# Kernel tuning notes

Hardware: AMD Instinct MI355X
Metric: run time of the kernel (lower is better)

The kernel has to match this reference:

```python
import jax, jax.numpy as jnp
import numpy as np
import math

D_MODEL = 512
HEADS = 8
GRID_COUNT = 40000
MAX_LEN = 5000


def _positional_embedding(d_model, max_len=MAX_LEN):
    pe = np.zeros((max_len, d_model), dtype=np.float32)
    position = np.arange(max_len, dtype=np.float32)[:, None]
    div_term = np.exp(np.arange(0, d_model, 2, dtype=np.float32) * -(math.log(10000.0) / d_model))
    pe[:, 0::2] = np.sin(position * div_term)
    pe[:, 1::2] = np.cos(position * div_term)
    return jnp.asarray(pe)  # [max_len, d_model]


def _mha(q, k, v, wq, bq, wk, bk, wv, bv, heads):
    # Faithful to SelfAttention: no 1/sqrt(d_k) scaling in the original.
    B, Sq, D = q.shape
    Sk = k.shape[1]
    dh = D // heads
    Q = (q @ wq.T + bq).reshape(B, Sq, heads, dh)
    K = (k @ wk.T + bk).reshape(B, Sk, heads, dh)
    V = (v @ wv.T + bv).reshape(B, Sk, heads, dh)
    attn = jax.nn.softmax(jnp.einsum('bqhd,bkhd->bhqk', Q, K), axis=-1)
    out = jnp.einsum('bhqk,bkhd->bqhd', attn, V)
    return out.reshape(B, Sq, D)


def setup_inputs() -> dict:
    key = jax.random.key(0)
    ks = jax.random.split(key, 20)
    B, S_CURR, S_HIST, N_MASK = 32, 128, 256, 16
    s = 1.0 / math.sqrt(D_MODEL)

    def lin(k):
        kw, kb = jax.random.split(k)
        w = jax.random.uniform(kw, (D_MODEL, D_MODEL), jnp.float32, -s, s)
        b = jax.random.uniform(kb, (D_MODEL,), jnp.float32, -s, s)
        return w, b

    h_wq, h_bq = lin(ks[0]); h_wk, h_bk = lin(ks[1]); h_wv, h_bv = lin(ks[2])
    c_wq, c_bq = lin(ks[3]); c_wk, c_bk = lin(ks[4]); c_wv, c_bv = lin(ks[5])
    x_wq, x_bq = lin(ks[6]); x_wk, x_bk = lin(ks[7]); x_wv, x_bv = lin(ks[8])
    t2_w, t2_b = lin(ks[9])
    emb = jax.random.normal(ks[10], (GRID_COUNT, D_MODEL), jnp.float32)

    return {
        'hist_traj_grid': jax.random.randint(ks[11], (B, S_HIST), 0, GRID_COUNT),
        'userId': jax.random.randint(ks[12], (B,), 0, 1000),
        'mask_pos': jax.random.randint(ks[13], (B, N_MASK), 0, S_CURR),
        'mask_curr_traj_grid': jax.random.randint(ks[14], (B, S_CURR), 0, GRID_COUNT),
        'aggregator_hist_traj_grid': jax.random.randint(ks[15], (B, S_HIST), 0, GRID_COUNT),
        'emb': emb,
        'h_wq': h_wq, 'h_bq': h_bq, 'h_wk': h_wk, 'h_bk': h_bk, 'h_wv': h_wv, 'h_bv': h_bv,
        'c_wq': c_wq, 'c_bq': c_bq, 'c_wk': c_wk, 'c_bk': c_bk, 'c_wv': c_wv, 'c_bv': c_bv,
        'x_wq': x_wq, 'x_bq': x_bq, 'x_wk': x_wk, 'x_bk': x_bk, 'x_wv': x_wv, 'x_bv': x_bv,
        't2_w': t2_w, 't2_b': t2_b,
    }


def reference(hist_traj_grid, userId, mask_pos, mask_curr_traj_grid, aggregator_hist_traj_grid,
              emb,
              h_wq, h_bq, h_wk, h_bk, h_wv, h_bv,
              c_wq, c_bq, c_wk, c_bk, c_wv, c_bv,
              x_wq, x_bq, x_wk, x_bk, x_wv, x_bv,
              t2_w, t2_b):
    pe = _positional_embedding(D_MODEL)
    hist = emb[aggregator_hist_traj_grid]          # [B, S_hist, D]
    curr = emb[mask_curr_traj_grid]                # [B, S_curr, D]
    hist = hist + pe[None, :hist.shape[1]]
    curr = curr + pe[None, :curr.shape[1]]

    hist = _mha(hist, hist, hist, h_wq, h_bq, h_wk, h_bk, h_wv, h_bv, HEADS)
    curr = _mha(curr, curr, curr, c_wq, c_bq, c_wk, c_bk, c_wv, c_bv, HEADS)
    _cross = _mha(curr, hist, hist, x_wq, x_bq, x_wk, x_bk, x_wv, x_bv, HEADS)
    # NOTE: original overwrites liner_transform output with liner_transform2(tanh(curr)),
    # so cross-attention output and liner_transform do not affect the result.
    hyb = jnp.tanh(curr) @ t2_w.T + t2_b           # [B, S_curr, D]

    # index_select of flattened [B*S, D] at mask_pos + b*S == take_along_axis over seq dim
    gathered = jnp.take_along_axis(hyb, mask_pos[:, :, None], axis=1)  # [B, n_mask, D]
    gathered = gathered.reshape(-1, D_MODEL)

    candidate = emb[2:]                            # [vocab-2, D]
    scores = gathered @ candidate.T                # [B*n_mask, vocab-2]
    return jax.nn.log_softmax(scores, axis=-1)
```

## Files before the change

### kernel.cpp

```cpp
#include <hip/hip_runtime.h>
#include <hip/hip_bf16.h>
#include <math.h>
#include <float.h>

#define B       32
#define S_CURR  128
#define D       512
#define H       8
#define DH      64
#define NM      16
#define NCAND   39998
#define MG      (B * NM)
#define SCLD    40064
#define NT      313

typedef __bf16 bf16x8_t __attribute__((ext_vector_type(8)));
typedef __bf16 bf16x4_t __attribute__((ext_vector_type(4)));
typedef __bf16 bf16x2_t __attribute__((ext_vector_type(2)));
typedef float  f32x4_t  __attribute__((ext_vector_type(4)));

typedef __attribute__((address_space(3))) unsigned int lds_u32_t;
typedef const __attribute__((address_space(1))) unsigned int gbl_u32_t;

__device__ __forceinline__ void async16(const void* g, void* l) {
    __builtin_amdgcn_global_load_lds((gbl_u32_t*)g, (lds_u32_t*)l, 16, 0, 0);
}

__global__ __launch_bounds__(256) void prep_kernel(
    const float* __restrict__ emb,
    const float* __restrict__ wq, const float* __restrict__ wk,
    const float* __restrict__ wv, const float* __restrict__ t2w,
    __bf16* __restrict__ embB, __bf16* __restrict__ wqB, __bf16* __restrict__ wkB,
    __bf16* __restrict__ wvB, __bf16* __restrict__ t2wB,
    const int* __restrict__ curr_idx, __bf16* __restrict__ currB,
    const int* __restrict__ mask_pos, int* __restrict__ qidx)
{
    int bx = blockIdx.x;
    if (bx < 10512) {
        const float* src; __bf16* dst; size_t n, base;
        if (bx < 10000) {
            src = emb + 2 * D; dst = embB; n = (size_t)NCAND * D; base = (size_t)bx * 2048;
        } else {
            int w = (bx - 10000) >> 7;
            base = (size_t)((bx - 10000) & 127) * 2048;
            n = (size_t)D * D;
            src = (w == 0) ? wq : (w == 1) ? wk : (w == 2) ? wv : t2w;
            dst = (w == 0) ? wqB : (w == 1) ? wkB : (w == 2) ? wvB : t2wB;
        }
        size_t i = base + (size_t)threadIdx.x * 8;
        if (i >= n) return;
        float4 a = *(const float4*)(src + i);
        float4 b = *(const float4*)(src + i + 4);
        bf16x8_t v;
        v[0] = (__bf16)a.x; v[1] = (__bf16)a.y; v[2] = (__bf16)a.z; v[3] = (__bf16)a.w;
        v[4] = (__bf16)b.x; v[5] = (__bf16)b.y; v[6] = (__bf16)b.z; v[7] = (__bf16)b.w;
        *(bf16x8_t*)(dst + i) = v;
        return;
    }
    if (bx == 14608) {
        int r = threadIdx.x;
        qidx[r] = (r >> 4) * S_CURR + mask_pos[r];
        r += 256;
        qidx[r] = (r >> 4) * S_CURR + mask_pos[r];
        return;
    }
    int bs = bx - 10512;
    int s = bs & (S_CURR - 1);
    int g = curr_idx[bs];
    const float* e = emb + (size_t)g * D;
    __bf16* o = currB + (size_t)bs * D;
    int d = threadIdx.x * 2;
    float div = __expf(-(float)d * (9.210340371976184f / 512.0f));
    float ang = (float)s * div;
    float2 ev = *(const float2*)(e + d);
    bf16x2_t ov;
    ov[0] = (__bf16)(ev.x + __sinf(ang));
    ov[1] = (__bf16)(ev.y + __cosf(ang));
    *(bf16x2_t*)(o + d) = ov;
}

__global__ __launch_bounds__(256) void gemm_bf(
    const __bf16* __restrict__ A,
    const __bf16* __restrict__ W0, const float* __restrict__ b0, __bf16* __restrict__ C0,
    const __bf16* __restrict__ W1, const float* __restrict__ b1, __bf16* __restrict__ C1,
    const __bf16* __restrict__ W2, const float* __restrict__ b2, __bf16* __restrict__ C2,
    const int* __restrict__ rowidx)
{
    const int z = blockIdx.z;
    if (z == 2 && blockIdx.x >= 4) return;
    const __bf16* W = (z == 0) ? W0 : (z == 1) ? W1 : W2;
    const float* bias = (z == 0) ? b0 : (z == 1) ? b1 : b2;
    __bf16* C = (z == 0) ? C0 : (z == 1) ? C1 : C2;

    __shared__ __bf16 As[2][128 * 64];
    __shared__ __bf16 Bs[2][128 * 64];

    const int tid = threadIdx.x, lane = tid & 63, wave = tid >> 6;
    const int wy = wave >> 1, wx = wave & 1;
    const int m0 = blockIdx.x * 128, n0 = blockIdx.y * 128;
    const int lrow = lane >> 3;
    const int lcol = (((lane & 7) ^ lrow) & 7) * 8;

    const __bf16* aptr[4]; const __bf16* bptr[4];
#pragma unroll
    for (int i = 0; i < 4; ++i) {
        int chunk = wave * 4 + i;
        int ar = m0 + chunk * 8 + lrow;
        if (z == 2) ar = rowidx[ar];
        aptr[i] = A + (size_t)ar * 512 + lcol;
        bptr[i] = W + (size_t)(n0 + chunk * 8 + lrow) * 512 + lcol;
    }

    f32x4_t acc[4][4];
#pragma unroll
    for (int i = 0; i < 4; ++i)
#pragma unroll
        for (int j = 0; j < 4; ++j) acc[i][j] = (f32x4_t){0.f, 0.f, 0.f, 0.f};

    const int l7 = lane & 7, quad = lane >> 4, c16 = lane & 15;

#pragma unroll
    for (int i = 0; i < 4; ++i) {
        int chunk = wave * 4 + i;
        async16(aptr[i], &As[0][chunk * 512]);
        async16(bptr[i], &Bs[0][chunk * 512]);
    }

#pragma unroll
    for (int t = 0; t < 8; ++t) {
        const int cur = t & 1;
        if (t < 7) {
            const int kk = (t + 1) * 64;
#pragma unroll
            for (int i = 0; i < 4; ++i) {
                int chunk = wave * 4 + i;
                async16(aptr[i] + kk, &As[cur ^ 1][chunk * 512]);
                async16(bptr[i] + kk, &Bs[cur ^ 1][chunk * 512]);
            }
            asm volatile("s_waitcnt vmcnt(8)" ::: "memory");
        } else {
            asm volatile("s_waitcnt vmcnt(0)" ::: "memory");
        }
        __builtin_amdgcn_s_barrier();
#pragma unroll
        for (int kb = 0; kb < 2; ++kb) {
            const int goff = (((kb * 4 + quad) ^ l7)) * 8;
            bf16x8_t af[4], bfv[4];
#pragma unroll
            for (int i = 0; i < 4; ++i)
                af[i] = *(const bf16x8_t*)&As[cur][(wy * 64 + i * 16 + c16) * 64 + goff];
#pragma unroll
            for (int j = 0; j < 4; ++j)
                bfv[j] = *(const bf16x8_t*)&Bs[cur][(wx * 64 + j * 16 + c16) * 64 + goff];
#pragma unroll
            for (int i = 0; i < 4; ++i)
#pragma unroll
                for (int j = 0; j < 4; ++j)
                    acc[i][j] = __builtin_amdgcn_mfma_f32_16x16x32_bf16(
                        bfv[j], af[i], acc[i][j], 0, 0, 0);
        }
        asm volatile("s_waitcnt lgkmcnt(0)" ::: "memory");
        __builtin_amdgcn_s_barrier();
    }

#pragma unroll
    for (int i = 0; i < 4; ++i) {
        const int row = m0 + wy * 64 + i * 16 + c16;
#pragma unroll
        for (int j = 0; j < 4; ++j) {
            const int colb = n0 + wx * 64 + j * 16 + quad * 4;
            float4 bv = *(const float4*)&bias[colb];
            bf16x4_t o;
            o[0] = (__bf16)(acc[i][j][0] + bv.x);
            o[1] = (__bf16)(acc[i][j][1] + bv.y);
            o[2] = (__bf16)(acc[i][j][2] + bv.z);
            o[3] = (__bf16)(acc[i][j][3] + bv.w);
            *(bf16x4_t*)&C[(size_t)row * 512 + colb] = o;
        }
    }
}

__global__ __launch_bounds__(256) void gemm_scores(
    const __bf16* __restrict__ A,
    const __bf16* __restrict__ Bm,
    __bf16* __restrict__ scB,
    float* __restrict__ pmax, float* __restrict__ psum)
{
    const int bid = blockIdx.x;
    const int xcd = bid & 7, k = bid >> 3;
    const int nt = xcd * 40 + (k >> 2);
    if (nt >= NT) return;
    const int m0 = (k & 3) * 128, n0 = nt * 128;

    __shared__ __bf16 As[2][128 * 32];
    __shared__ __bf16 Bs[2][128 * 32];
    __shared__ float redm[2][128], reds[2][128];

    const int tid = threadIdx.x, lane = tid & 63, wave = tid >> 6;
    const int wy = wave >> 1, wx = wave & 1;
    const int lrow16 = lane >> 2;
    const int pos    = lane & 3;
    const int quad = lane >> 4, c16 = lane & 15;

    const __bf16* aptr[2]; const __bf16* bptr[2]; int ldso[2];
#pragma unroll
    for (int i = 0; i < 2; ++i) {
        const int c = wave * 2 + i;
        const int g = pos ^ (lrow16 & 3) ^ (lrow16 >> 2);
        aptr[i] = A  + (size_t)(m0 + c * 16 + lrow16) * 512 + g * 8;
        bptr[i] = Bm + (size_t)(n0 + c * 16 + lrow16) * 512 + g * 8;
        ldso[i] = c * 512;
    }

    f32x4_t acc[4][4];
#pragma unroll
    for (int i = 0; i < 4; ++i)
#pragma unroll
        for (int j = 0; j < 4; ++j) acc[i][j] = (f32x4_t){0.f, 0.f, 0.f, 0.f};

#pragma unroll
    for (int i = 0; i < 2; ++i) {
        async16(aptr[i], &As[0][ldso[i]]);
        async16(bptr[i], &Bs[0][ldso[i]]);
    }

    const int goff = ((quad ^ (c16 & 3) ^ (c16 >> 2))) * 8;

#pragma unroll
    for (int t = 0; t < 16; ++t) {
        const int cur = t & 1;
        if (t < 15) {
            const int kk = (t + 1) * 32;
#pragma unroll
            for (int i = 0; i < 2; ++i) {
                async16(aptr[i] + kk, &As[cur ^ 1][ldso[i]]);
                async16(bptr[i] + kk, &Bs[cur ^ 1][ldso[i]]);
            }
            asm volatile("s_waitcnt vmcnt(4)" ::: "memory");
        } else {
            asm volatile("s_waitcnt vmcnt(0)" ::: "memory");
        }
        __builtin_amdgcn_s_barrier();
        bf16x8_t af[4], bfv[4];
#pragma unroll
        for (int i = 0; i < 4; ++i)
            af[i] = *(const bf16x8_t*)&As[cur][(wy * 64 + i * 16 + c16) * 32 + goff];
#pragma unroll
        for (int j = 0; j < 4; ++j)
            bfv[j] = *(const bf16x8_t*)&Bs[cur][(wx * 64 + j * 16 + c16) * 32 + goff];
#pragma unroll
        for (int i = 0; i < 4; ++i)
#pragma unroll
            for (int j = 0; j < 4; ++j)
                acc[i][j] = __builtin_amdgcn_mfma_f32_16x16x32_bf16(
                    bfv[j], af[i], acc[i][j], 0, 0, 0);
        asm volatile("s_waitcnt lgkmcnt(0)" ::: "memory");
        __builtin_amdgcn_s_barrier();
    }

    const bool tailb = (n0 + 128 > NCAND);
#pragma unroll
    for (int i = 0; i < 4; ++i) {
        const int lrw = wy * 64 + i * 16 + c16;
        const size_t rowbase = (size_t)(m0 + lrw) * SCLD;
        float vs[4][4];
        float vmax = -FLT_MAX;
        float ssum = 0.f;
        if (!tailb) {
#pragma unroll
            for (int j = 0; j < 4; ++j) {
                const int nb = n0 + wx * 64 + j * 16 + quad * 4;
                bf16x4_t o;
#pragma unroll
                for (int rr = 0; rr < 4; ++rr) {
                    __bf16 xb = (__bf16)acc[i][j][rr];
                    o[rr] = xb;
                    float xr = (float)xb;
                    vs[j][rr] = xr;
                    vmax = fmaxf(vmax, xr);
                }
                *(bf16x4_t*)&scB[rowbase + nb] = o;
            }
#pragma unroll
            for (int j = 0; j < 4; ++j)
#pragma unroll
                for (int rr = 0; rr < 4; ++rr)
                    ssum += __expf(vs[j][rr] - vmax);
        } else {
            for (int j = 0; j < 4; ++j) {
                const int nb = n0 + wx * 64 + j * 16 + quad * 4;
                for (int rr = 0; rr < 4; ++rr) {
                    const int n = nb + rr;
                    __bf16 xb = (__bf16)acc[i][j][rr];
                    float xr = (float)xb;
                    if (n < NCAND) {
                        scB[rowbase + n] = xb;
                        vs[j][rr] = xr;
                        vmax = fmaxf(vmax, xr);
                    } else vs[j][rr] = -FLT_MAX;
                }
            }
            for (int j = 0; j < 4; ++j)
                for (int rr = 0; rr < 4; ++rr)
                    ssum += (vs[j][rr] > -FLT_MAX) ? __expf(vs[j][rr] - vmax) : 0.f;
        }
#pragma unroll
        for (int mk = 16; mk < 64; mk <<= 1) {
            float om = __shfl_xor(vmax, mk);
            float os = __shfl_xor(ssum, mk);
            float mm = fmaxf(vmax, om);
            ssum = ssum * __expf(vmax - mm) + os * __expf(om - mm);
            vmax = mm;
        }
        if (quad == 0) { redm[wx][lrw] = vmax; reds[wx][lrw] = ssum; }
    }
    __syncthreads();
    if (tid < 128) {
        float ma = redm[0][tid], sa = reds[0][tid];
        float mb = redm[1][tid], sb = reds[1][tid];
        float mm = fmaxf(ma, mb);
        float ss = sa * __expf(ma - mm) + sb * __expf(mb - mm);
        pmax[(size_t)(m0 + tid) * NT + nt] = mm;
        psum[(size_t)(m0 + tid) * NT + nt] = ss;
    }
}

#define KPAD 72
__global__ __launch_bounds__(256) void attn_kernel(const __bf16* __restrict__ Qg,
                                                   const __bf16* __restrict__ K,
                                                   const __bf16* __restrict__ V,
                                                   __bf16* __restrict__ attnB) {
    const int b = blockIdx.x, h = blockIdx.y, t = threadIdx.x;
    __shared__ __bf16 Ks[128 * KPAD];
    __shared__ __bf16 Vs[128 * KPAD];
    __shared__ float  Qs[16 * 68];
    __shared__ float  P[16 * 130];

    for (int i = t; i < 1024; i += 256) {
        int row = i >> 3, cg = (i & 7) * 8;
        size_t gsrc = ((size_t)(b * S_CURR + row)) * D + h * DH + cg;
        *(bf16x8_t*)&Ks[row * KPAD + cg] = *(const bf16x8_t*)&K[gsrc];
        *(bf16x8_t*)&Vs[row * KPAD + cg] = *(const bf16x8_t*)&V[gsrc];
    }
    if (t < 128) {
        int q = t >> 3, cg = (t & 7) * 8;
        bf16x8_t qv = *(const bf16x8_t*)&Qg[((size_t)(b * NM + q)) * D + h * DH + cg];
#pragma unroll
        for (int u = 0; u < 8; ++u) Qs[q * 68 + cg + u] = (float)qv[u];
    }
    __syncthreads();

    const int q = t >> 4, i = t & 15;
    float sv[8];
    float lmax = -FLT_MAX;
#pragma unroll
    for (int z = 0; z < 8; ++z) {
        int kk = i + z * 16;
        float s = 0.f;
#pragma unroll
        for (int d0 = 0; d0 < DH; d0 += 8) {
            bf16x8_t kv = *(const bf16x8_t*)&Ks[kk * KPAD + d0];
#pragma unroll
            for (int u = 0; u < 8; ++u) s += Qs[q * 68 + d0 + u] * (float)kv[u];
        }
        sv[z] = s; lmax = fmaxf(lmax, s);
    }
#pragma unroll
    for (int mk = 1; mk < 16; mk <<= 1) lmax = fmaxf(lmax, __shfl_xor(lmax, mk));
    float lsum = 0.f;
#pragma unroll
    for (int z = 0; z < 8; ++z) {
        float e = __expf(sv[z] - lmax);
        P[q * 130 + i + z * 16] = e;
        lsum += e;
    }
#pragma unroll
    for (int mk = 1; mk < 16; mk <<= 1) lsum += __shfl_xor(lsum, mk);
    const float inv = 1.0f / lsum;

    const int d = i * 4;
    float a0 = 0.f, a1 = 0.f, a2 = 0.f, a3 = 0.f;
    for (int kk = 0; kk < 128; ++kk) {
        float p = P[q * 130 + kk];
        bf16x4_t vv = *(const bf16x4_t*)&Vs[kk * KPAD + d];
        a0 += p * (float)vv[0]; a1 += p * (float)vv[1];
        a2 += p * (float)vv[2]; a3 += p * (float)vv[3];
    }
    __bf16* o = attnB + ((size_t)(b * NM + q)) * D + h * DH + d;
    o[0] = (__bf16)tanhf(a0 * inv); o[1] = (__bf16)tanhf(a1 * inv);
    o[2] = (__bf16)tanhf(a2 * inv); o[3] = (__bf16)tanhf(a3 * inv);
}

__global__ __launch_bounds__(256) void lse_final(const float* __restrict__ pmax,
                                                 const float* __restrict__ psum,
                                                 const __bf16* __restrict__ scB,
                                                 float* __restrict__ out) {
    const int row = blockIdx.x, t = threadIdx.x;
    __shared__ float ms[256], ss[256];
    float m = -FLT_MAX, s = 0.f;
    for (int i = t; i < NT; i += 256) {
        float om = pmax[(size_t)row * NT + i];
        float os = psum[(size_t)row * NT + i];
        float mm = fmaxf(m, om);
        s = s * __expf(m - mm) + os * __expf(om - mm);
        m = mm;
    }
    ms[t] = m; ss[t] = s;
    __syncthreads();
    for (int off = 128; off > 0; off >>= 1) {
        if (t < off) {
            float m1 = ms[t], s1 = ss[t], m2 = ms[t + off], s2 = ss[t + off];
            float mm = fmaxf(m1, m2);
            ms[t] = mm;
            ss[t] = s1 * __expf(m1 - mm) + s2 * __expf(m2 - mm);
        }
        __syncthreads();
    }
    const float l = ms[0] + logf(ss[0]);

    const __bf16* src = scB + (size_t)row * SCLD;
    float* o = out + (size_t)row * NCAND;
    for (int c0 = t * 8; c0 < NCAND; c0 += 256 * 8) {
        bf16x8_t v = *(const bf16x8_t*)(src + c0);
        if (c0 + 8 <= NCAND) {
            *(float2*)(o + c0)     = make_float2((float)v[0] - l, (float)v[1] - l);
            *(float2*)(o + c0 + 2) = make_float2((float)v[2] - l, (float)v[3] - l);
            *(float2*)(o + c0 + 4) = make_float2((float)v[4] - l, (float)v[5] - l);
            *(float2*)(o + c0 + 6) = make_float2((float)v[6] - l, (float)v[7] - l);
        } else {
            for (int k2 = 0; k2 < NCAND - c0; ++k2) o[c0 + k2] = (float)v[k2] - l;
        }
    }
}

extern "C" void kernel_launch(void* const* d_in, const int* in_sizes, int n_in,
                              void* d_out, int out_size, void* d_ws, size_t ws_size,
                              hipStream_t stream) {
    const int*   mask_pos = (const int*)d_in[2];
    const int*   curr_idx = (const int*)d_in[3];
    const float* emb      = (const float*)d_in[5];
    const float* c_wq = (const float*)d_in[12];
    const float* c_bq = (const float*)d_in[13];
    const float* c_wk = (const float*)d_in[14];
    const float* c_bk = (const float*)d_in[15];
    const float* c_wv = (const float*)d_in[16];
    const float* c_bv = (const float*)d_in[17];
    const float* t2_w = (const float*)d_in[24];
    const float* t2_b = (const float*)d_in[25];
    float* out = (float*)d_out;

    char* w = (char*)d_ws;
    __bf16* embB  = (__bf16*)w;
    __bf16* scB   = (__bf16*)(w + 41025536);
    __bf16* currB = scB;
    __bf16* Kf    = (__bf16*)(w + 41025536 + 4194304);
    __bf16* Vf    = (__bf16*)(w + 41025536 + 8388608);
    __bf16* Qg    = (__bf16*)(w + 41025536 + 12582912);
    __bf16* attnB = (__bf16*)(w + 41025536 + 13107200);
    __bf16* wqB   = (__bf16*)(w + 41025536 + 13631488);
    __bf16* wkB   = (__bf16*)(w + 41025536 + 14155776);
    __bf16* wvB   = (__bf16*)(w + 41025536 + 14680064);
    __bf16* t2wB  = (__bf16*)(w + 41025536 + 15204352);
    int*    qidx  = (int*)   (w + 41025536 + 15728640);
    __bf16* gatheredB = (__bf16*)(w + 82051072);
    float*  pmax  = (float*)(w + 82575360);
    float*  psum  = (float*)(w + 83216384);

    hipLaunchKernelGGL(prep_kernel, dim3(14609), dim3(256), 0, stream,
                       emb, c_wq, c_wk, c_wv, t2_w, embB, wqB, wkB, wvB, t2wB,
                       curr_idx, currB, mask_pos, qidx);
    hipLaunchKernelGGL(gemm_bf, dim3(32, 4, 3), dim3(256), 0, stream,
                       currB, wkB, c_bk, Kf, wvB, c_bv, Vf, wqB, c_bq, Qg, qidx);
    hipLaunchKernelGGL(attn_kernel, dim3(B, H), dim3(256), 0, stream,
                       Qg, Kf, Vf, attnB);
    hipLaunchKernelGGL(gemm_bf, dim3(4, 4, 1), dim3(256), 0, stream,
                       attnB, t2wB, t2_b, gatheredB,
                       t2wB, t2_b, gatheredB, t2wB, t2_b, gatheredB,
                       (const int*)nullptr);
    hipLaunchKernelGGL(gemm_scores, dim3(1280), dim3(256), 0, stream,
                       gatheredB, embB, scB, pmax, psum);
    hipLaunchKernelGGL(lse_final, dim3(MG), dim3(256), 0, stream,
                       pmax, psum, scB, out);
}
```

Baseline: 289.7 us.

## Fuse fp32-to-bf16 embedding conversion into the scores GEMM B-tile loads

The separate prep pass that converted the whole 40k x 512 embedding table to bf16 is removed. The scores GEMM now reads fp32 embedding rows straight from global memory into registers, converts them to bf16 and writes them into LDS, prefetching one k-step ahead. This drops a full write and re-read of the bf16 table, roughly 41 MB each way. In exchange, each GEMM block reads twice as many bytes for B, and the direct async LDS loads for B become register loads plus LDS stores, which lengthens the inner loop's pipeline.

```diff
diff --git a/kernel.cpp b/kernel.cpp
--- a/kernel.cpp
+++ b/kernel.cpp
@@ -30,25 +30,18 @@
     const float* __restrict__ emb,
     const float* __restrict__ wq, const float* __restrict__ wk,
     const float* __restrict__ wv, const float* __restrict__ t2w,
-    __bf16* __restrict__ embB, __bf16* __restrict__ wqB, __bf16* __restrict__ wkB,
+    __bf16* __restrict__ wqB, __bf16* __restrict__ wkB,
     __bf16* __restrict__ wvB, __bf16* __restrict__ t2wB,
     const int* __restrict__ curr_idx, __bf16* __restrict__ currB,
     const int* __restrict__ mask_pos, int* __restrict__ qidx)
 {
     int bx = blockIdx.x;
-    if (bx < 10512) {
-        const float* src; __bf16* dst; size_t n, base;
-        if (bx < 10000) {
-            src = emb + 2 * D; dst = embB; n = (size_t)NCAND * D; base = (size_t)bx * 2048;
-        } else {
-            int w = (bx - 10000) >> 7;
-            base = (size_t)((bx - 10000) & 127) * 2048;
-            n = (size_t)D * D;
-            src = (w == 0) ? wq : (w == 1) ? wk : (w == 2) ? wv : t2w;
-            dst = (w == 0) ? wqB : (w == 1) ? wkB : (w == 2) ? wvB : t2wB;
-        }
+    if (bx < 512) {
+        int w = bx >> 7;
+        size_t base = (size_t)(bx & 127) * 2048;
+        const float* src = (w == 0) ? wq : (w == 1) ? wk : (w == 2) ? wv : t2w;
+        __bf16* dst = (w == 0) ? wqB : (w == 1) ? wkB : (w == 2) ? wvB : t2wB;
         size_t i = base + (size_t)threadIdx.x * 8;
-        if (i >= n) return;
         float4 a = *(const float4*)(src + i);
         float4 b = *(const float4*)(src + i + 4);
         bf16x8_t v;
@@ -57,14 +50,14 @@
         *(bf16x8_t*)(dst + i) = v;
         return;
     }
-    if (bx == 14608) {
+    if (bx == 4608) {
         int r = threadIdx.x;
         qidx[r] = (r >> 4) * S_CURR + mask_pos[r];
         r += 256;
         qidx[r] = (r >> 4) * S_CURR + mask_pos[r];
         return;
     }
-    int bs = bx - 10512;
+    int bs = bx - 512;
     int s = bs & (S_CURR - 1);
     int g = curr_idx[bs];
     const float* e = emb + (size_t)g * D;
@@ -182,7 +175,7 @@
 
 __global__ __launch_bounds__(256) void gemm_scores(
     const __bf16* __restrict__ A,
-    const __bf16* __restrict__ Bm,
+    const float* __restrict__ emb2,
     __bf16* __restrict__ scB,
     float* __restrict__ pmax, float* __restrict__ psum)
 {
@@ -201,15 +194,18 @@
     const int lrow16 = lane >> 2;
     const int pos    = lane & 3;
     const int quad = lane >> 4, c16 = lane & 15;
-
-    const __bf16* aptr[2]; const __bf16* bptr[2]; int ldso[2];
+    const int g = pos ^ (lrow16 & 3) ^ (lrow16 >> 2);
+
+    const __bf16* aptr[2]; const float* bptr[2]; int aldso[2], bldso[2];
 #pragma unroll
     for (int i = 0; i < 2; ++i) {
         const int c = wave * 2 + i;
-        const int g = pos ^ (lrow16 & 3) ^ (lrow16 >> 2);
-        aptr[i] = A  + (size_t)(m0 + c * 16 + lrow16) * 512 + g * 8;
-        bptr[i] = Bm + (size_t)(n0 + c * 16 + lrow16) * 512 + g * 8;
-        ldso[i] = c * 512;
+        aptr[i]  = A + (size_t)(m0 + c * 16 + lrow16) * 512 + g * 8;
+        int brow = n0 + c * 16 + lrow16;
+        if (brow >= NCAND) brow = NCAND - 1;
+        bptr[i]  = emb2 + (size_t)brow * 512 + g * 8;
+        aldso[i] = c * 512;
+        bldso[i] = c * 512 + lrow16 * 32 + pos * 8;
     }
 
     f32x4_t acc[4][4];
@@ -218,11 +214,33 @@
 #pragma unroll
         for (int j = 0; j < 4; ++j) acc[i][j] = (f32x4_t){0.f, 0.f, 0.f, 0.f};
 
+    float4 rb[2][2];
 #pragma unroll
     for (int i = 0; i < 2; ++i) {
-        async16(aptr[i], &As[0][ldso[i]]);
-        async16(bptr[i], &Bs[0][ldso[i]]);
-    }
+        rb[i][0] = *(const float4*)(bptr[i]);
+        rb[i][1] = *(const float4*)(bptr[i] + 4);
+    }
+#pragma unroll
+    for (int i = 0; i < 2; ++i)
+        async16(aptr[i], &As[0][aldso[i]]);
+    asm volatile("s_waitcnt vmcnt(2)" ::: "memory");
+#pragma unroll
+    for (int i = 0; i < 2; ++i) {
+        bf16x8_t bw;
+        bw[0] = (__bf16)rb[i][0].x; bw[1] = (__bf16)rb[i][0].y;
+        bw[2] = (__bf16)rb[i][0].z; bw[3] = (__bf16)rb[i][0].w;
+        bw[4] = (__bf16)rb[i][1].x; bw[5] = (__bf16)rb[i][1].y;
+        bw[6] = (__bf16)rb[i][1].z; bw[7] = (__bf16)rb[i][1].w;
+        *(bf16x8_t*)&Bs[0][bldso[i]] = bw;
+    }
+#pragma unroll
+    for (int i = 0; i < 2; ++i) {
+        rb[i][0] = *(const float4*)(bptr[i] + 32);
+        rb[i][1] = *(const float4*)(bptr[i] + 36);
+    }
+    asm volatile("s_waitcnt vmcnt(4)" ::: "memory");
+    asm volatile("s_waitcnt lgkmcnt(0)" ::: "memory");
+    __builtin_amdgcn_s_barrier();
 
     const int goff = ((quad ^ (c16 & 3) ^ (c16 >> 2))) * 8;
 
@@ -230,17 +248,27 @@
     for (int t = 0; t < 16; ++t) {
         const int cur = t & 1;
         if (t < 15) {
-            const int kk = (t + 1) * 32;
+#pragma unroll
+            for (int i = 0; i < 2; ++i)
+                async16(aptr[i] + (t + 1) * 32, &As[cur ^ 1][aldso[i]]);
+            asm volatile("s_waitcnt vmcnt(2)" ::: "memory");
 #pragma unroll
             for (int i = 0; i < 2; ++i) {
-                async16(aptr[i] + kk, &As[cur ^ 1][ldso[i]]);
-                async16(bptr[i] + kk, &Bs[cur ^ 1][ldso[i]]);
+                bf16x8_t bw;
+                bw[0] = (__bf16)rb[i][0].x; bw[1] = (__bf16)rb[i][0].y;
+                bw[2] = (__bf16)rb[i][0].z; bw[3] = (__bf16)rb[i][0].w;
+                bw[4] = (__bf16)rb[i][1].x; bw[5] = (__bf16)rb[i][1].y;
+                bw[6] = (__bf16)rb[i][1].z; bw[7] = (__bf16)rb[i][1].w;
+                *(bf16x8_t*)&Bs[cur ^ 1][bldso[i]] = bw;
             }
-            asm volatile("s_waitcnt vmcnt(4)" ::: "memory");
-        } else {
-            asm volatile("s_waitcnt vmcnt(0)" ::: "memory");
-        }
-        __builtin_amdgcn_s_barrier();
+            if (t < 14) {
+#pragma unroll
+                for (int i = 0; i < 2; ++i) {
+                    rb[i][0] = *(const float4*)(bptr[i] + (t + 2) * 32);
+                    rb[i][1] = *(const float4*)(bptr[i] + (t + 2) * 32 + 4);
+                }
+            }
+        }
         bf16x8_t af[4], bfv[4];
 #pragma unroll
         for (int i = 0; i < 4; ++i)
@@ -254,6 +282,8 @@
             for (int j = 0; j < 4; ++j)
                 acc[i][j] = __builtin_amdgcn_mfma_f32_16x16x32_bf16(
                     bfv[j], af[i], acc[i][j], 0, 0, 0);
+        if (t < 14)      asm volatile("s_waitcnt vmcnt(4)" ::: "memory");
+        else if (t == 14) asm volatile("s_waitcnt vmcnt(0)" ::: "memory");
         asm volatile("s_waitcnt lgkmcnt(0)" ::: "memory");
         __builtin_amdgcn_s_barrier();
     }
@@ -450,7 +480,6 @@
     float* out = (float*)d_out;
 
     char* w = (char*)d_ws;
-    __bf16* embB  = (__bf16*)w;
     __bf16* scB   = (__bf16*)(w + 41025536);
     __bf16* currB = scB;
     __bf16* Kf    = (__bf16*)(w + 41025536 + 4194304);
@@ -466,8 +495,8 @@
     float*  pmax  = (float*)(w + 82575360);
     float*  psum  = (float*)(w + 83216384);
 
-    hipLaunchKernelGGL(prep_kernel, dim3(14609), dim3(256), 0, stream,
-                       emb, c_wq, c_wk, c_wv, t2_w, embB, wqB, wkB, wvB, t2wB,
+    hipLaunchKernelGGL(prep_kernel, dim3(4609), dim3(256), 0, stream,
+                       emb, c_wq, c_wk, c_wv, t2_w, wqB, wkB, wvB, t2wB,
                        curr_idx, currB, mask_pos, qidx);
     hipLaunchKernelGGL(gemm_bf, dim3(32, 4, 3), dim3(256), 0, stream,
                        currB, wkB, c_bk, Kf, wvB, c_bv, Vf, wqB, c_bq, Qg, qidx);
@@ -478,7 +507,7 @@
                        t2wB, t2_b, gatheredB, t2wB, t2_b, gatheredB,
                        (const int*)nullptr);
     hipLaunchKernelGGL(gemm_scores, dim3(1280), dim3(256), 0, stream,
-                       gatheredB, embB, scB, pmax, psum);
+                       gatheredB, emb + 2 * D, scB, pmax, psum);
     hipLaunchKernelGGL(lse_final, dim3(MG), dim3(256), 0, stream,
                        pmax, psum, scB, out);
 }
```

Result: faster. 283.9 us (-2.0%).
